# Kernel tuning notes

Hardware: AMD Instinct MI355X
Metric: run time of the kernel (lower is better)

The kernel has to match this reference:

```python
import jax, jax.numpy as jnp
import numpy as np


def setup_inputs() -> dict:
    key = jax.random.key(0)
    ks = jax.random.split(key, 7)
    S, A, I, H = 2000, 1000, 5, 32
    return {
        "g": jax.random.normal(ks[0], (S, A, I), dtype=jnp.float32),
        "W1": jax.random.normal(ks[1], (A, I, H), dtype=jnp.float32) * (1.0 / np.sqrt(I)),
        "b1": jax.random.normal(ks[2], (A, H), dtype=jnp.float32) * 0.01,
        "W2": jax.random.normal(ks[3], (A, H, H), dtype=jnp.float32) * (1.0 / np.sqrt(H)),
        "b2": jax.random.normal(ks[4], (A, H), dtype=jnp.float32) * 0.01,
        "W3": jax.random.normal(ks[5], (A, H, 1), dtype=jnp.float32) * (1.0 / np.sqrt(H)),
        "b3": jax.random.normal(ks[6], (A, 1), dtype=jnp.float32) * 0.01,
    }


def reference(g, W1, b1, W2, b2, W3, b3):
    # Batched equivalent of the nested per-struct / per-atom Python loop:
    # each atom `a` has its own tiny MLP (5 -> 32 -> 32 -> 1, tanh),
    # applied to g[s, a] for every structure s. Grouped-GEMM form:
    # s = struct, a = atom, i/h/o = feature dims.
    h1 = jnp.tanh(jnp.einsum('sai,aih->sah', g, W1) + b1[None, :, :])
    h2 = jnp.tanh(jnp.einsum('sah,aho->sao', h1, W2) + b2[None, :, :])
    e = jnp.einsum('sah,aho->sao', h2, W3) + b3[None, :, :]
    # e_nn has shape [n_struct, n_atoms], matching the torch buffer.
    return e[..., 0]
```

## Files before the change

### kernel.cpp

```cpp
#include <hip/hip_runtime.h>
#include <hip/hip_bf16.h>

#define NS_TOT 2000
#define NA 1000
#define NI 5
#define NH 32
#define SHALF 1000

typedef __attribute__((ext_vector_type(2)))  float f32x2;
typedef __attribute__((ext_vector_type(8)))  short short8;
typedef __attribute__((ext_vector_type(16))) float f32x16;

struct f4pair  { f32x2 a, b; };
struct accpair { f32x2 p[8]; };

__device__ __forceinline__ float fast_tanh(float x) {
    float z = x * x;
    float n = fmaf(z + 105.0f, z, 945.0f);
    float d = fmaf(fmaf(z, 15.0f, 420.0f), z, 945.0f);
    float r = __builtin_amdgcn_rcpf(d);
    float tv = x * n * r;
    return __builtin_amdgcn_fmed3f(tv, -1.0f, 1.0f);
}
__device__ __forceinline__ f32x2 tanh_pk(f32x2 X) {
    f32x2 z = X * X;
    f32x2 n = (z + 105.0f) * z + 945.0f;
    f32x2 d = (z * 15.0f + 420.0f) * z + 945.0f;
    f32x2 r;
    r.x = __builtin_amdgcn_rcpf(d.x);
    r.y = __builtin_amdgcn_rcpf(d.y);
    f32x2 t = X * n * r;
    t.x = __builtin_amdgcn_fmed3f(t.x, -1.0f, 1.0f);
    t.y = __builtin_amdgcn_fmed3f(t.y, -1.0f, 1.0f);
    return t;
}

__device__ __forceinline__ unsigned short f2bf_rne(float x) {
    unsigned u = __float_as_uint(x);
    unsigned r = u + 0x7FFFu + ((u >> 16) & 1u);
    return (unsigned short)(r >> 16);
}
__device__ __forceinline__ unsigned pack2(float a, float b) {
    __hip_bfloat162 p = __float22bfloat162_rn(make_float2(a, b));
    unsigned u; __builtin_memcpy(&u, &p, 4); return u;
}

__global__ __attribute__((amdgpu_flat_work_group_size(256, 256),
                          amdgpu_waves_per_eu(4, 4)))
void mlp_mfma(
    const float* __restrict__ g,
    const float* __restrict__ W1, const float* __restrict__ b1,
    const float* __restrict__ W2, const float* __restrict__ b2,
    const float* __restrict__ W3, const float* __restrict__ b3,
    float* __restrict__ out)
{
    const int bid   = blockIdx.x;
    const int araw  = bid % NA;
    const int chunk = bid / NA;
    const int a = (araw >> 3) + 125 * (araw & 7);
    const int t = threadIdx.x;
    const int lane = t & 63, wid = t >> 6;
    const int l31 = lane & 31, half = lane >> 5;

    const int sbase_blk = chunk * SHALF;
    const int send      = sbase_blk + SHALF;

    __shared__ __align__(16) unsigned short sW2T[NH * NH];
    __shared__ __align__(16) unsigned short sW1T[NH * 8];
    __shared__ __align__(16) float sB2[NH];
    __shared__ __align__(16) float sW3[NH];

    for (int idx = t; idx < NH * NH; idx += 256) {
        const int i = idx >> 5, j = idx & 31;
        sW2T[j * NH + i] = f2bf_rne(W2[(size_t)a * NH * NH + idx]);
    }
    if (t < NH) {
        sB2[t] = b2[a * NH + t];
        sW3[t] = W3[a * NH + t];
        const int m = t;
        #pragma unroll
        for (int i = 0; i < NI; ++i)
            sW1T[m * 8 + i] = f2bf_rne(W1[(size_t)a * NI * NH + i * NH + m]);
        sW1T[m * 8 + 5] = f2bf_rne(b1[a * NH + m]);
        sW1T[m * 8 + 6] = 0;
        sW1T[m * 8 + 7] = 0;
    }
    __syncthreads();

    const short8 zero8 = {0,0,0,0,0,0,0,0};
    const short8 w1ld = __builtin_bit_cast(short8, *(const uint4*)(sW1T + l31 * 8));
    const short8 afl1 = half ? zero8 : w1ld;
    const short8 af0 = __builtin_bit_cast(short8, *(const uint4*)(sW2T + l31 * NH + half * 8));
    const short8 af1 = __builtin_bit_cast(short8, *(const uint4*)(sW2T + l31 * NH + 16 + half * 8));
    const float4 b2q0 = ((const float4*)sB2)[0 + half];
    const float4 b2q1 = ((const float4*)sB2)[2 + half];
    const float4 b2q2 = ((const float4*)sB2)[4 + half];
    const float4 b2q3 = ((const float4*)sB2)[6 + half];
    const float4 w3q0 = ((const float4*)sW3)[0 + half];
    const float4 w3q1 = ((const float4*)sW3)[2 + half];
    const float4 w3q2 = ((const float4*)sW3)[4 + half];
    const float4 w3q3 = ((const float4*)sW3)[6 + half];
    const float bias3 = b3[a];
    const f4pair w3p0 = __builtin_bit_cast(f4pair, w3q0);
    const f4pair w3p1 = __builtin_bit_cast(f4pair, w3q1);
    const f4pair w3p2 = __builtin_bit_cast(f4pair, w3q2);
    const f4pair w3p3 = __builtin_bit_cast(f4pair, w3q3);
    const f32x16 zacc = {0,0,0,0,0,0,0,0,0,0,0,0,0,0,0,0};

    for (int it = 0; it < 4; ++it) {
        const int base = sbase_blk + it * 256 + wid * 64;
        const int s = base + lane;
        const int sl = (s < send) ? s : (send - 1);

        const float* gp = g + ((size_t)sl * NA + a) * NI;
        const float x0g = gp[0], x1g = gp[1], x2g = gp[2], x3g = gp[3], x4g = gp[4];

        const unsigned gp01 = pack2(x0g, x1g);
        const unsigned gp23 = pack2(x2g, x3g);
        const unsigned gp45 = pack2(x4g, 1.0f);
        const unsigned q01 = __shfl_xor((int)gp01, 32);
        const unsigned q23 = __shfl_xor((int)gp23, 32);
        const unsigned q45 = __shfl_xor((int)gp45, 32);
        const unsigned zu = 0;
        uint4 bu0 = make_uint4(half ? zu : gp01, half ? zu : gp23,
                               half ? zu : gp45, zu);
        uint4 bu1 = make_uint4(half ? zu : q01, half ? zu : q23,
                               half ? zu : q45, zu);
        const short8 gb0 = __builtin_bit_cast(short8, bu0);
        const short8 gb1 = __builtin_bit_cast(short8, bu1);

        f32x16 d0 = __builtin_amdgcn_mfma_f32_32x32x16_bf16(afl1, gb0, zacc, 0, 0, 0);
        f32x16 d1 = __builtin_amdgcn_mfma_f32_32x32x16_bf16(afl1, gb1, zacc, 0, 0, 0);

        short8 bk0_0, bk1_0, bk0_1, bk1_1;
        #define TILE_CONV(DD, BK0, BK1) { \
            float th[16]; \
            th[0]=fast_tanh(DD[0]);   th[1]=fast_tanh(DD[1]); \
            th[2]=fast_tanh(DD[2]);   th[3]=fast_tanh(DD[3]); \
            th[4]=fast_tanh(DD[4]);   th[5]=fast_tanh(DD[5]); \
            th[6]=fast_tanh(DD[6]);   th[7]=fast_tanh(DD[7]); \
            th[8]=fast_tanh(DD[8]);   th[9]=fast_tanh(DD[9]); \
            th[10]=fast_tanh(DD[10]); th[11]=fast_tanh(DD[11]); \
            th[12]=fast_tanh(DD[12]); th[13]=fast_tanh(DD[13]); \
            th[14]=fast_tanh(DD[14]); th[15]=fast_tanh(DD[15]); \
            float rc[8]; \
            rc[0] = __shfl_xor(half ? th[0]  : th[4],  32); \
            rc[1] = __shfl_xor(half ? th[1]  : th[5],  32); \
            rc[2] = __shfl_xor(half ? th[2]  : th[6],  32); \
            rc[3] = __shfl_xor(half ? th[3]  : th[7],  32); \
            rc[4] = __shfl_xor(half ? th[8]  : th[12], 32); \
            rc[5] = __shfl_xor(half ? th[9]  : th[13], 32); \
            rc[6] = __shfl_xor(half ? th[10] : th[14], 32); \
            rc[7] = __shfl_xor(half ? th[11] : th[15], 32); \
            float e0[8], e1[8]; \
            e0[0] = half ? rc[0] : th[0]; e0[1] = half ? rc[1] : th[1]; \
            e0[2] = half ? rc[2] : th[2]; e0[3] = half ? rc[3] : th[3]; \
            e0[4] = half ? th[4] : rc[0]; e0[5] = half ? th[5] : rc[1]; \
            e0[6] = half ? th[6] : rc[2]; e0[7] = half ? th[7] : rc[3]; \
            e1[0] = half ? rc[4] : th[8];  e1[1] = half ? rc[5] : th[9]; \
            e1[2] = half ? rc[6] : th[10]; e1[3] = half ? rc[7] : th[11]; \
            e1[4] = half ? th[12] : rc[4]; e1[5] = half ? th[13] : rc[5]; \
            e1[6] = half ? th[14] : rc[6]; e1[7] = half ? th[15] : rc[7]; \
            uint4 u0 = make_uint4(pack2(e0[0],e0[1]), pack2(e0[2],e0[3]), \
                                  pack2(e0[4],e0[5]), pack2(e0[6],e0[7])); \
            uint4 u1 = make_uint4(pack2(e1[0],e1[1]), pack2(e1[2],e1[3]), \
                                  pack2(e1[4],e1[5]), pack2(e1[6],e1[7])); \
            BK0 = __builtin_bit_cast(short8, u0); \
            BK1 = __builtin_bit_cast(short8, u1); }
        TILE_CONV(d0, bk0_0, bk1_0)
        TILE_CONV(d1, bk0_1, bk1_1)
        #undef TILE_CONV

        f32x16 acc0 = {b2q0.x, b2q0.y, b2q0.z, b2q0.w,
                       b2q1.x, b2q1.y, b2q1.z, b2q1.w,
                       b2q2.x, b2q2.y, b2q2.z, b2q2.w,
                       b2q3.x, b2q3.y, b2q3.z, b2q3.w};
        f32x16 acc1 = acc0;
        acc0 = __builtin_amdgcn_mfma_f32_32x32x16_bf16(af0, bk0_0, acc0, 0, 0, 0);
        acc0 = __builtin_amdgcn_mfma_f32_32x32x16_bf16(af1, bk1_0, acc0, 0, 0, 0);
        acc1 = __builtin_amdgcn_mfma_f32_32x32x16_bf16(af0, bk0_1, acc1, 0, 0, 0);
        acc1 = __builtin_amdgcn_mfma_f32_32x32x16_bf16(af1, bk1_1, acc1, 0, 0, 0);

        const accpair ap0 = __builtin_bit_cast(accpair, acc0);
        const accpair ap1 = __builtin_bit_cast(accpair, acc1);
        f32x2 p0 = {0.f, 0.f}, p1 = {0.f, 0.f};
        #define EPP(r, wpair) { \
            p0 += tanh_pk(ap0.p[r]) * (wpair); \
            p1 += tanh_pk(ap1.p[r]) * (wpair); }
        EPP(0, w3p0.a) EPP(1, w3p0.b)
        EPP(2, w3p1.a) EPP(3, w3p1.b)
        EPP(4, w3p2.a) EPP(5, w3p2.b)
        EPP(6, w3p3.a) EPP(7, w3p3.b)
        #undef EPP
        float e0 = p0.x + p0.y;
        float e1 = p1.x + p1.y;
        e0 += __shfl_xor(e0, 32);
        e1 += __shfl_xor(e1, 32);

        if (lane < 32) {
            const int st0 = base + l31;
            const int st1 = base + 32 + l31;
            if (st0 < send) out[(size_t)st0 * NA + a] = e0 + bias3;
            if (st1 < send) out[(size_t)st1 * NA + a] = e1 + bias3;
        }
    }
}

extern "C" void kernel_launch(void* const* d_in, const int* in_sizes, int n_in,
                              void* d_out, int out_size, void* d_ws, size_t ws_size,
                              hipStream_t stream) {
    const float* g  = (const float*)d_in[0];
    const float* W1 = (const float*)d_in[1];
    const float* b1 = (const float*)d_in[2];
    const float* W2 = (const float*)d_in[3];
    const float* b2 = (const float*)d_in[4];
    const float* W3 = (const float*)d_in[5];
    const float* b3 = (const float*)d_in[6];
    float* out = (float*)d_out;
    mlp_mfma<<<dim3(NA * 2), dim3(256), 0, stream>>>(g, W1, b1, W2, b2, W3, b3, out);
}
```

Measured before the change: 127.4 us.

## Prefetch next g tile and replace shuffles with permlane32_swap

Software-pipelines the per-iteration load of g by fetching the next iteration's inputs before computing the current one, and fully unrolls the loop. Replaces ds_bpermute-based __shfl_xor half-wave exchanges and select chains with the gfx950 permlane32_swap instruction in the input packing, the tanh-to-bf16 repack, and the final reduction. It also hoists the bias accumulator init and lets all 64 lanes store results. The changes add register pressure from the prefetched values and unrolling, and depend on the swap ordering matching the old MFMA operand layout.

```diff
diff --git a/kernel.cpp b/kernel.cpp
--- a/kernel.cpp
+++ b/kernel.cpp
@@ -106,26 +106,40 @@
     const f4pair w3p2 = __builtin_bit_cast(f4pair, w3q2);
     const f4pair w3p3 = __builtin_bit_cast(f4pair, w3q3);
     const f32x16 zacc = {0,0,0,0,0,0,0,0,0,0,0,0,0,0,0,0};
-
+    const f32x16 b2acc = {b2q0.x, b2q0.y, b2q0.z, b2q0.w,
+                          b2q1.x, b2q1.y, b2q1.z, b2q1.w,
+                          b2q2.x, b2q2.y, b2q2.z, b2q2.w,
+                          b2q3.x, b2q3.y, b2q3.z, b2q3.w};
+
+    float x0g, x1g, x2g, x3g, x4g;
+    {
+        const int s0 = sbase_blk + wid * 64 + lane;
+        const int sl = (s0 < send) ? s0 : (send - 1);
+        const float* gp = g + ((size_t)sl * NA + a) * NI;
+        x0g = gp[0]; x1g = gp[1]; x2g = gp[2]; x3g = gp[3]; x4g = gp[4];
+    }
+
+    #pragma unroll
     for (int it = 0; it < 4; ++it) {
         const int base = sbase_blk + it * 256 + wid * 64;
         const int s = base + lane;
-        const int sl = (s < send) ? s : (send - 1);
-
-        const float* gp = g + ((size_t)sl * NA + a) * NI;
-        const float x0g = gp[0], x1g = gp[1], x2g = gp[2], x3g = gp[3], x4g = gp[4];
+
+        float nx0, nx1, nx2, nx3, nx4;
+        if (it < 3) {
+            const int sn = s + 256;
+            const int sln = (sn < send) ? sn : (send - 1);
+            const float* gq = g + ((size_t)sln * NA + a) * NI;
+            nx0 = gq[0]; nx1 = gq[1]; nx2 = gq[2]; nx3 = gq[3]; nx4 = gq[4];
+        }
 
         const unsigned gp01 = pack2(x0g, x1g);
         const unsigned gp23 = pack2(x2g, x3g);
         const unsigned gp45 = pack2(x4g, 1.0f);
-        const unsigned q01 = __shfl_xor((int)gp01, 32);
-        const unsigned q23 = __shfl_xor((int)gp23, 32);
-        const unsigned q45 = __shfl_xor((int)gp45, 32);
-        const unsigned zu = 0;
-        uint4 bu0 = make_uint4(half ? zu : gp01, half ? zu : gp23,
-                               half ? zu : gp45, zu);
-        uint4 bu1 = make_uint4(half ? zu : q01, half ? zu : q23,
-                               half ? zu : q45, zu);
+        auto gs01 = __builtin_amdgcn_permlane32_swap(gp01, gp01, false, false);
+        auto gs23 = __builtin_amdgcn_permlane32_swap(gp23, gp23, false, false);
+        auto gs45 = __builtin_amdgcn_permlane32_swap(gp45, gp45, false, false);
+        const uint4 bu0 = make_uint4(gp01,    gp23,    gp45,    0u);
+        const uint4 bu1 = make_uint4(gs01[1], gs23[1], gs45[1], 0u);
         const short8 gb0 = __builtin_bit_cast(short8, bu0);
         const short8 gb1 = __builtin_bit_cast(short8, bu1);
 
@@ -134,51 +148,29 @@
 
         short8 bk0_0, bk1_0, bk0_1, bk1_1;
         #define TILE_CONV(DD, BK0, BK1) { \
-            float th[16]; \
-            th[0]=fast_tanh(DD[0]);   th[1]=fast_tanh(DD[1]); \
-            th[2]=fast_tanh(DD[2]);   th[3]=fast_tanh(DD[3]); \
-            th[4]=fast_tanh(DD[4]);   th[5]=fast_tanh(DD[5]); \
-            th[6]=fast_tanh(DD[6]);   th[7]=fast_tanh(DD[7]); \
-            th[8]=fast_tanh(DD[8]);   th[9]=fast_tanh(DD[9]); \
-            th[10]=fast_tanh(DD[10]); th[11]=fast_tanh(DD[11]); \
-            th[12]=fast_tanh(DD[12]); th[13]=fast_tanh(DD[13]); \
-            th[14]=fast_tanh(DD[14]); th[15]=fast_tanh(DD[15]); \
-            float rc[8]; \
-            rc[0] = __shfl_xor(half ? th[0]  : th[4],  32); \
-            rc[1] = __shfl_xor(half ? th[1]  : th[5],  32); \
-            rc[2] = __shfl_xor(half ? th[2]  : th[6],  32); \
-            rc[3] = __shfl_xor(half ? th[3]  : th[7],  32); \
-            rc[4] = __shfl_xor(half ? th[8]  : th[12], 32); \
-            rc[5] = __shfl_xor(half ? th[9]  : th[13], 32); \
-            rc[6] = __shfl_xor(half ? th[10] : th[14], 32); \
-            rc[7] = __shfl_xor(half ? th[11] : th[15], 32); \
-            float e0[8], e1[8]; \
-            e0[0] = half ? rc[0] : th[0]; e0[1] = half ? rc[1] : th[1]; \
-            e0[2] = half ? rc[2] : th[2]; e0[3] = half ? rc[3] : th[3]; \
-            e0[4] = half ? th[4] : rc[0]; e0[5] = half ? th[5] : rc[1]; \
-            e0[6] = half ? th[6] : rc[2]; e0[7] = half ? th[7] : rc[3]; \
-            e1[0] = half ? rc[4] : th[8];  e1[1] = half ? rc[5] : th[9]; \
-            e1[2] = half ? rc[6] : th[10]; e1[3] = half ? rc[7] : th[11]; \
-            e1[4] = half ? th[12] : rc[4]; e1[5] = half ? th[13] : rc[5]; \
-            e1[6] = half ? th[14] : rc[6]; e1[7] = half ? th[15] : rc[7]; \
-            uint4 u0 = make_uint4(pack2(e0[0],e0[1]), pack2(e0[2],e0[3]), \
-                                  pack2(e0[4],e0[5]), pack2(e0[6],e0[7])); \
-            uint4 u1 = make_uint4(pack2(e1[0],e1[1]), pack2(e1[2],e1[3]), \
-                                  pack2(e1[4],e1[5]), pack2(e1[6],e1[7])); \
+            const unsigned p0 = pack2(fast_tanh(DD[0]),  fast_tanh(DD[1])); \
+            const unsigned p1 = pack2(fast_tanh(DD[2]),  fast_tanh(DD[3])); \
+            const unsigned p2 = pack2(fast_tanh(DD[4]),  fast_tanh(DD[5])); \
+            const unsigned p3 = pack2(fast_tanh(DD[6]),  fast_tanh(DD[7])); \
+            const unsigned p4 = pack2(fast_tanh(DD[8]),  fast_tanh(DD[9])); \
+            const unsigned p5 = pack2(fast_tanh(DD[10]), fast_tanh(DD[11])); \
+            const unsigned p6 = pack2(fast_tanh(DD[12]), fast_tanh(DD[13])); \
+            const unsigned p7 = pack2(fast_tanh(DD[14]), fast_tanh(DD[15])); \
+            auto s02 = __builtin_amdgcn_permlane32_swap(p0, p2, false, false); \
+            auto s13 = __builtin_amdgcn_permlane32_swap(p1, p3, false, false); \
+            auto s46 = __builtin_amdgcn_permlane32_swap(p4, p6, false, false); \
+            auto s57 = __builtin_amdgcn_permlane32_swap(p5, p7, false, false); \
+            const uint4 u0 = make_uint4(s02[0], s13[0], s02[1], s13[1]); \
+            const uint4 u1 = make_uint4(s46[0], s57[0], s46[1], s57[1]); \
             BK0 = __builtin_bit_cast(short8, u0); \
             BK1 = __builtin_bit_cast(short8, u1); }
         TILE_CONV(d0, bk0_0, bk1_0)
         TILE_CONV(d1, bk0_1, bk1_1)
         #undef TILE_CONV
 
-        f32x16 acc0 = {b2q0.x, b2q0.y, b2q0.z, b2q0.w,
-                       b2q1.x, b2q1.y, b2q1.z, b2q1.w,
-                       b2q2.x, b2q2.y, b2q2.z, b2q2.w,
-                       b2q3.x, b2q3.y, b2q3.z, b2q3.w};
-        f32x16 acc1 = acc0;
-        acc0 = __builtin_amdgcn_mfma_f32_32x32x16_bf16(af0, bk0_0, acc0, 0, 0, 0);
+        f32x16 acc0 = __builtin_amdgcn_mfma_f32_32x32x16_bf16(af0, bk0_0, b2acc, 0, 0, 0);
         acc0 = __builtin_amdgcn_mfma_f32_32x32x16_bf16(af1, bk1_0, acc0, 0, 0, 0);
-        acc1 = __builtin_amdgcn_mfma_f32_32x32x16_bf16(af0, bk0_1, acc1, 0, 0, 0);
+        f32x16 acc1 = __builtin_amdgcn_mfma_f32_32x32x16_bf16(af0, bk0_1, b2acc, 0, 0, 0);
         acc1 = __builtin_amdgcn_mfma_f32_32x32x16_bf16(af1, bk1_1, acc1, 0, 0, 0);
 
         const accpair ap0 = __builtin_bit_cast(accpair, acc0);
@@ -192,17 +184,15 @@
         EPP(4, w3p2.a) EPP(5, w3p2.b)
         EPP(6, w3p3.a) EPP(7, w3p3.b)
         #undef EPP
-        float e0 = p0.x + p0.y;
-        float e1 = p1.x + p1.y;
-        e0 += __shfl_xor(e0, 32);
-        e1 += __shfl_xor(e1, 32);
-
-        if (lane < 32) {
-            const int st0 = base + l31;
-            const int st1 = base + 32 + l31;
-            if (st0 < send) out[(size_t)st0 * NA + a] = e0 + bias3;
-            if (st1 < send) out[(size_t)st1 * NA + a] = e1 + bias3;
-        }
+        const float e0 = p0.x + p0.y;
+        const float e1 = p1.x + p1.y;
+        auto es = __builtin_amdgcn_permlane32_swap(__float_as_uint(e0),
+                                                   __float_as_uint(e1),
+                                                   false, false);
+        const float etot = __uint_as_float(es[0]) + __uint_as_float(es[1]);
+        if (s < send) out[(size_t)s * NA + a] = etot + bias3;
+
+        if (it < 3) { x0g = nx0; x1g = nx1; x2g = nx2; x3g = nx3; x4g = nx4; }
     }
 }
 
```

Result: faster. 124.8 us (-2.1%).
